# Kernel tuning notes

Hardware: AMD Instinct MI355X
Metric: run time of the kernel (lower is better)

Reference implementation:

```python
import jax, jax.numpy as jnp
import numpy as np

NUM_HEADS = 12


def setup_inputs() -> dict:
    key = jax.random.key(0)
    ks = jax.random.split(key, 7)
    B, H, W, C = 1, 64, 64, 768
    hd = C // NUM_HEADS
    return {
        "x": jax.random.normal(ks[0], (B, H, W, C), dtype=jnp.float32),
        "qkv_w": jax.random.normal(ks[1], (C, 3 * C), dtype=jnp.float32) * 0.02,
        "qkv_b": jax.random.normal(ks[2], (3 * C,), dtype=jnp.float32) * 0.02,
        "proj_w": jax.random.normal(ks[3], (C, C), dtype=jnp.float32) * 0.02,
        "proj_b": jax.random.normal(ks[4], (C,), dtype=jnp.float32) * 0.02,
        "rel_pos_h": jax.random.normal(ks[5], (2 * H - 1, hd), dtype=jnp.float32) * 0.02,
        "rel_pos_w": jax.random.normal(ks[6], (2 * W - 1, hd), dtype=jnp.float32) * 0.02,
    }


def _rel_table(size, rel_pos):
    # q_size == k_size so relative_coords = i - j + (size - 1)
    coords = jnp.arange(size)[:, None] - jnp.arange(size)[None, :] + (size - 1)
    return rel_pos[coords]  # [size, size, head_dim]


def reference(x, qkv_w, qkv_b, proj_w, proj_b, rel_pos_h, rel_pos_w):
    B, H, W, C = x.shape
    nh = NUM_HEADS
    hd = C // nh
    scale = hd ** -0.5
    N = H * W

    qkv = x.reshape(B, N, C) @ qkv_w + qkv_b  # [B, N, 3C]
    qkv = qkv.reshape(B, N, 3, nh, hd).transpose(2, 0, 3, 1, 4).reshape(3, B * nh, N, hd)
    q, k, v = qkv[0], qkv[1], qkv[2]

    attn = jnp.einsum("bqd,bkd->bqk", q * scale, k)  # [B*nh, N, N]

    # decomposed relative position bias
    Rh = _rel_table(H, rel_pos_h)  # [H, H, hd]
    Rw = _rel_table(W, rel_pos_w)  # [W, W, hd]
    qr = q.reshape(B * nh, H, W, hd)
    rel_h = jnp.einsum("bhwc,hkc->bhwk", qr, Rh)  # [B*nh, H, W, H]
    rel_w = jnp.einsum("bhwc,wkc->bhwk", qr, Rw)  # [B*nh, H, W, W]
    bias = rel_h[..., :, None] + rel_w[..., None, :]  # [B*nh, H, W, H, W]
    attn = attn + bias.reshape(B * nh, N, N)

    attn = jax.nn.softmax(attn, axis=-1)
    out = jnp.einsum("bqk,bkd->bqd", attn, v)  # [B*nh, N, hd]
    out = out.reshape(B, nh, H, W, hd).transpose(0, 2, 3, 1, 4).reshape(B, H, W, C)
    return out @ proj_w + proj_b
```

## Files before the change

### kernel.cpp

```cpp
#include <hip/hip_runtime.h>
#include <math.h>

#define NHEADS 12
#define NTOK 4096
#define LOG2E 1.44269504f

typedef __attribute__((ext_vector_type(8))) short bf8v;
typedef __attribute__((ext_vector_type(4))) float f4v;
typedef __attribute__((ext_vector_type(16))) float f16v;

__device__ __forceinline__ unsigned short f2bf(float f) {
  unsigned int u = __float_as_uint(f);
  u += 0x7fffu + ((u >> 16) & 1u);
  return (unsigned short)(u >> 16);
}
__device__ __forceinline__ float bf2f(unsigned short h) {
  return __uint_as_float(((unsigned int)h) << 16);
}
__device__ __forceinline__ bf8v pack8(float4 a, float4 b) {
  bf8v v;
  v[0] = (short)f2bf(a.x); v[1] = (short)f2bf(a.y);
  v[2] = (short)f2bf(a.z); v[3] = (short)f2bf(a.w);
  v[4] = (short)f2bf(b.x); v[5] = (short)f2bf(b.y);
  v[6] = (short)f2bf(b.z); v[7] = (short)f2bf(b.w);
  return v;
}
__device__ __forceinline__ unsigned pkbf(float hi, float lo) {
  return __builtin_amdgcn_perm(__float_as_uint(hi) + 0x8000u,
                               __float_as_uint(lo) + 0x8000u, 0x07060302u);
}

__global__ __launch_bounds__(256) void cvt_kernel(
    const float* __restrict__ in, short* __restrict__ out)
{
    const size_t i = ((size_t)blockIdx.x * 256 + threadIdx.x) * 8;
    float4 a = *(const float4*)(in + i);
    float4 b = *(const float4*)(in + i + 4);
    *(bf8v*)(out + i) = pack8(a, b);
}

__global__ __launch_bounds__(256) void cvt_rpw_kernel(
    const float* __restrict__ in, short* __restrict__ out)
{
    const int idx = blockIdx.x * 256 + threadIdx.x;
    const float v = (idx < 127 * 64) ? in[idx] : 0.f;
    out[idx] = (short)f2bf(v);
}

__global__ __launch_bounds__(256) void tcvt_kernel(
    const float* __restrict__ in, short* __restrict__ out, int R, int C)
{
    __shared__ float Ts[64][65];
    const int bc = blockIdx.x * 64, br = blockIdx.y * 64, t = threadIdx.x;
    {
        const int r = t >> 2, c0 = (t & 3) * 16;
        const float* src = in + (size_t)(br + r) * C + bc + c0;
#pragma unroll
        for (int i = 0; i < 4; ++i) {
            float4 a = *(const float4*)(src + 4 * i);
            Ts[r][c0 + 4 * i + 0] = a.x;
            Ts[r][c0 + 4 * i + 1] = a.y;
            Ts[r][c0 + 4 * i + 2] = a.z;
            Ts[r][c0 + 4 * i + 3] = a.w;
        }
    }
    __syncthreads();
    const int c = t >> 2, r0 = (t & 3) * 16;
    short* dst = out + (size_t)(bc + c) * R + br + r0;
#pragma unroll
    for (int p = 0; p < 2; ++p) {
        bf8v v;
#pragma unroll
        for (int i = 0; i < 8; ++i) v[i] = (short)f2bf(Ts[r0 + p * 8 + i][c]);
        *(bf8v*)(dst + p * 8) = v;
    }
}

__device__ __forceinline__ void gload_lds16(const void* g, void* l) {
  __builtin_amdgcn_global_load_lds(
      (const __attribute__((address_space(1))) void*)g,
      (__attribute__((address_space(3))) void*)l, 16, 0, 0);
}

__global__ __launch_bounds__(256) void qkv_mfma_kernel(
    const short* __restrict__ xh, const short* __restrict__ wT,
    const float* __restrict__ bias, short* __restrict__ qbh,
    short* __restrict__ kbh, short* __restrict__ vbT)
{
    __shared__ __align__(16) short As[128 * 32];
    __shared__ __align__(16) short Bs[128 * 32];
    const int t = threadIdx.x;
    const int w = t >> 6, lane = t & 63;
    const int l15 = lane & 15, l4 = lane >> 4;
    const int wr = w >> 1, wc = w & 1;
    const int row0 = blockIdx.y * 128, col0 = blockIdx.x * 128;
    const int ldr = lane >> 2;
    const int ldk = (lane & 3) * 8;

    f4v acc[4][4] = {};
    const short* aBase = xh + (size_t)(row0 + w * 32 + ldr) * 768 + ldk;
    const short* bBase = wT + (size_t)(col0 + w * 32 + ldr) * 768 + ldk;

    for (int kk = 0; kk < 768; kk += 32) {
        __syncthreads();
#pragma unroll
        for (int c = 0; c < 2; ++c) {
            gload_lds16(aBase + (size_t)c * 16 * 768 + kk,
                        &As[(w * 32 + c * 16) * 32]);
            gload_lds16(bBase + (size_t)c * 16 * 768 + kk,
                        &Bs[(w * 32 + c * 16) * 32]);
        }
        __syncthreads();
        bf8v af[4], bg[4];
#pragma unroll
        for (int i = 0; i < 4; ++i) {
            af[i] = *(const bf8v*)&As[(wr * 64 + 16 * i + l15) * 32 + l4 * 8];
            bg[i] = *(const bf8v*)&Bs[(wc * 64 + 16 * i + l15) * 32 + l4 * 8];
        }
#pragma unroll
        for (int i = 0; i < 4; ++i)
#pragma unroll
            for (int j = 0; j < 4; ++j)
                acc[i][j] = __builtin_amdgcn_mfma_f32_16x16x32_bf16(
                    af[i], bg[j], acc[i][j], 0, 0, 0);
    }

#pragma unroll
    for (int j = 0; j < 4; ++j) {
        const int n = col0 + wc * 64 + 16 * j + l15;
        const int s = n / 768;
        const int rm = n - s * 768;
        const int h = rm >> 6, d = rm & 63;
        const float bv = bias[n];
        if (s == 2) {
            short* vdst = vbT + (size_t)(h * 64 + d) * NTOK;
#pragma unroll
            for (int i = 0; i < 4; ++i) {
                const int m = row0 + wr * 64 + 16 * i + l4 * 4;
                short4 pv;
                pv.x = (short)f2bf(acc[i][j][0] + bv);
                pv.y = (short)f2bf(acc[i][j][1] + bv);
                pv.z = (short)f2bf(acc[i][j][2] + bv);
                pv.w = (short)f2bf(acc[i][j][3] + bv);
                *(short4*)(vdst + m) = pv;
            }
        } else {
            short* dst = (s == 0) ? qbh : kbh;
#pragma unroll
            for (int i = 0; i < 4; ++i) {
                const int m = row0 + wr * 64 + 16 * i + l4 * 4;
#pragma unroll
                for (int r = 0; r < 4; ++r)
                    dst[((size_t)h * NTOK + m + r) * 64 + d] =
                        (short)f2bf(acc[i][j][r] + bv);
            }
        }
    }
}

__global__ __launch_bounds__(256) void relu_kernel(
    const short* __restrict__ qbh, const short* __restrict__ rpwb,
    short* __restrict__ rWb)
{
    __shared__ float Us[128][65];
    const int h = blockIdx.x, qh = blockIdx.y;
    const int t = threadIdx.x, w = t >> 6, lane = t & 63;
    const int l15 = lane & 15, l4 = lane >> 4;
    const size_t hB = (size_t)h * NTOK * 64;

    bf8v bq[4][2];
#pragma unroll
    for (int nt = 0; nt < 4; ++nt) {
        const short* qs = qbh + hB + (size_t)(qh * 64 + nt * 16 + l15) * 64;
#pragma unroll
        for (int s = 0; s < 2; ++s)
            bq[nt][s] = *(const bf8v*)(qs + s * 32 + l4 * 8);
    }
    bf8v aw[2][2];
#pragma unroll
    for (int mi = 0; mi < 2; ++mi) {
        const short* as = rpwb + (size_t)((w * 2 + mi) * 16 + l15) * 64;
#pragma unroll
        for (int s = 0; s < 2; ++s)
            aw[mi][s] = *(const bf8v*)(as + s * 32 + l4 * 8);
    }
    f4v U[2][4] = {};
#pragma unroll
    for (int mi = 0; mi < 2; ++mi)
#pragma unroll
        for (int nt = 0; nt < 4; ++nt)
#pragma unroll
            for (int s = 0; s < 2; ++s)
                U[mi][nt] = __builtin_amdgcn_mfma_f32_16x16x32_bf16(
                    aw[mi][s], bq[nt][s], U[mi][nt], 0, 0, 0);
#pragma unroll
    for (int mi = 0; mi < 2; ++mi)
#pragma unroll
        for (int nt = 0; nt < 4; ++nt)
#pragma unroll
            for (int r = 0; r < 4; ++r)
                Us[(w * 2 + mi) * 16 + l4 * 4 + r][nt * 16 + l15] =
                    U[mi][nt][r];
    __syncthreads();
    const int kw = t & 63, q0 = t >> 6;
#pragma unroll
    for (int i = 0; i < 16; ++i) {
        const int q = q0 * 16 + i;
        rWb[hB + (size_t)(qh * 64 + q) * 64 + kw] =
            (short)f2bf(Us[q + 63 - kw][q] * LOG2E);
    }
}

__global__ __launch_bounds__(256, 3) void flash_mfma_kernel(
    const short* __restrict__ qbh, const short* __restrict__ kbh,
    const short* __restrict__ vbT, const short* __restrict__ rWb,
    const float* __restrict__ rph, short* __restrict__ aob)
{
    __shared__ __align__(16) short Ks[128][68];
    __shared__ __align__(16) short Vt[64][132];
    __shared__ float relHs[64][65];

    const int t = threadIdx.x;
    const int qt = blockIdx.x, head = blockIdx.y;
    const int row0 = qt * 64;
    const int lane = t & 63, w = t >> 6;
    const int qh2 = w & 1, th = w >> 1;
    const int l31 = lane & 31, hf = lane >> 5;
    const size_t hB = (size_t)head * NTOK * 64;
    const float SC = 0.125f * LOG2E;

    const int q = row0 + qh2 * 32 + l31;
    bf8v bQ[4];
    {
        const short* qsrc = qbh + hB + (size_t)q * 64;
#pragma unroll
        for (int ks = 0; ks < 4; ++ks)
            bQ[ks] = *(const bf8v*)(qsrc + ks * 16 + hf * 8);
    }
    uint2 rwp[2][4];
    {
        const short* rsrc = rWb + hB + (size_t)q * 64;
#pragma unroll
        for (int t32 = 0; t32 < 2; ++t32)
#pragma unroll
            for (int g = 0; g < 4; ++g)
                rwp[t32][g] =
                    *(const uint2*)(rsrc + t32 * 32 + 8 * g + 4 * hf);
    }

    {
        const int rr = t >> 2, d0 = (t & 3) * 16;
        const float* src = rph + (size_t)(qt + 63 - rr) * 64 + d0;
        float4 a0 = *(const float4*)(src);
        float4 a1 = *(const float4*)(src + 4);
        float4 a2 = *(const float4*)(src + 8);
        float4 a3 = *(const float4*)(src + 12);
        a0.x *= LOG2E; a0.y *= LOG2E; a0.z *= LOG2E; a0.w *= LOG2E;
        a1.x *= LOG2E; a1.y *= LOG2E; a1.z *= LOG2E; a1.w *= LOG2E;
        a2.x *= LOG2E; a2.y *= LOG2E; a2.z *= LOG2E; a2.w *= LOG2E;
        a3.x *= LOG2E; a3.y *= LOG2E; a3.z *= LOG2E; a3.w *= LOG2E;
        *(bf8v*)&Ks[rr][d0] = pack8(a0, a1);
        *(bf8v*)&Ks[rr][d0 + 8] = pack8(a2, a3);
    }
    const int sx = t >> 2;
    const int sck = (t & 3) * 16;
    const int scv = (t & 3) * 32;
    const short* kptr = kbh + hB + (size_t)sx * 64 + sck;
    const short* vptr = vbT + ((size_t)head * 64 + sx) * NTOK + scv;
    bf8v kpf[4], vpf[4];
    kpf[0] = *(const bf8v*)(kptr);
    kpf[1] = *(const bf8v*)(kptr + 8);
    kpf[2] = *(const bf8v*)(kptr + 64 * 64);
    kpf[3] = *(const bf8v*)(kptr + 64 * 64 + 8);
    vpf[0] = *(const bf8v*)(vptr);
    vpf[1] = *(const bf8v*)(vptr + 8);
    vpf[2] = *(const bf8v*)(vptr + 16);
    vpf[3] = *(const bf8v*)(vptr + 24);

    __syncthreads();
    {
        f16v c = {};
#pragma unroll
        for (int ks = 0; ks < 4; ++ks)
            c = __builtin_amdgcn_mfma_f32_32x32x16_bf16(
                *(const bf8v*)&Ks[th * 32 + l31][ks * 16 + hf * 8], bQ[ks],
                c, 0, 0, 0);
#pragma unroll
        for (int reg = 0; reg < 16; ++reg)
            relHs[th * 32 + (reg & 3) + 8 * (reg >> 2) + 4 * hf]
                 [qh2 * 32 + l31] = c[reg];
    }

    f16v O[2] = {{}, {}};
    float lsum = 0.f;

    for (int it = 0; it < 32; ++it) {
        __syncthreads();
        *(bf8v*)&Ks[sx][sck] = kpf[0];
        *(bf8v*)&Ks[sx][sck + 8] = kpf[1];
        *(bf8v*)&Ks[sx + 64][sck] = kpf[2];
        *(bf8v*)&Ks[sx + 64][sck + 8] = kpf[3];
        *(bf8v*)&Vt[sx][scv] = vpf[0];
        *(bf8v*)&Vt[sx][scv + 8] = vpf[1];
        *(bf8v*)&Vt[sx][scv + 16] = vpf[2];
        *(bf8v*)&Vt[sx][scv + 24] = vpf[3];
        {
            const int itn = (it < 31) ? it + 1 : 31;
            const short* kp = kptr + (size_t)itn * 128 * 64;
            const short* vp = vptr + itn * 128;
            kpf[0] = *(const bf8v*)kp;
            kpf[1] = *(const bf8v*)(kp + 8);
            kpf[2] = *(const bf8v*)(kp + 64 * 64);
            kpf[3] = *(const bf8v*)(kp + 64 * 64 + 8);
            vpf[0] = *(const bf8v*)vp;
            vpf[1] = *(const bf8v*)(vp + 8);
            vpf[2] = *(const bf8v*)(vp + 16);
            vpf[3] = *(const bf8v*)(vp + 24);
        }
        __syncthreads();

        f16v acc[2] = {{}, {}};
#pragma unroll
        for (int ks = 0; ks < 4; ++ks)
#pragma unroll
            for (int t32 = 0; t32 < 2; ++t32)
                acc[t32] = __builtin_amdgcn_mfma_f32_32x32x16_bf16(
                    *(const bf8v*)&Ks[th * 64 + t32 * 32 + l31]
                                     [ks * 16 + hf * 8],
                    bQ[ks], acc[t32], 0, 0, 0);

        const float rh = relHs[2 * it + th][qh2 * 32 + l31];

        unsigned xg[2][4], yg[2][4];
#pragma unroll
        for (int t32 = 0; t32 < 2; ++t32) {
            float sub = 0.f;
#pragma unroll
            for (int g = 0; g < 4; ++g) {
                const unsigned u0 = rwp[t32][g].x;
                const unsigned u1 = rwp[t32][g].y;
                const float b0 = __uint_as_float(u0 << 16) + rh;
                const float b1 = __uint_as_float(u0 & 0xffff0000u) + rh;
                const float b2 = __uint_as_float(u1 << 16) + rh;
                const float b3 = __uint_as_float(u1 & 0xffff0000u) + rh;
                const float e0 = __builtin_amdgcn_exp2f(
                    fmaf(acc[t32][4 * g + 0], SC, b0));
                const float e1 = __builtin_amdgcn_exp2f(
                    fmaf(acc[t32][4 * g + 1], SC, b1));
                const float e2 = __builtin_amdgcn_exp2f(
                    fmaf(acc[t32][4 * g + 2], SC, b2));
                const float e3 = __builtin_amdgcn_exp2f(
                    fmaf(acc[t32][4 * g + 3], SC, b3));
                sub += (e0 + e1) + (e2 + e3);
                xg[t32][g] = pkbf(e1, e0);
                yg[t32][g] = pkbf(e3, e2);
            }
            lsum += sub;
        }

#pragma unroll
        for (int t32 = 0; t32 < 2; ++t32)
#pragma unroll
            for (int ks2 = 0; ks2 < 2; ++ks2) {
                auto px = __builtin_amdgcn_permlane32_swap(
                    xg[t32][2 * ks2], xg[t32][2 * ks2 + 1], false, false);
                auto py = __builtin_amdgcn_permlane32_swap(
                    yg[t32][2 * ks2], yg[t32][2 * ks2 + 1], false, false);
                int4 av;
                av.x = (int)px[0];
                av.y = (int)py[0];
                av.z = (int)px[1];
                av.w = (int)py[1];
                union { int4 i; bf8v v; } u; u.i = av;
#pragma unroll
                for (int nt = 0; nt < 2; ++nt)
                    O[nt] = __builtin_amdgcn_mfma_f32_32x32x16_bf16(
                        u.v,
                        *(const bf8v*)&Vt[nt * 32 + l31]
                                         [th * 64 + t32 * 32 + ks2 * 16 +
                                          hf * 8],
                        O[nt], 0, 0, 0);
            }
    }

    lsum += __shfl_xor(lsum, 32);
    float* OEp = (float*)&Ks[0][0];
    float* lEp = (float*)&Vt[0][0];
    __syncthreads();
    if (th == 1) {
#pragma unroll
        for (int nt = 0; nt < 2; ++nt)
#pragma unroll
            for (int reg = 0; reg < 16; ++reg) {
                const int qr = (reg & 3) + 8 * (reg >> 2) + 4 * hf;
                OEp[(size_t)(qh2 * 32 + qr) * 64 + nt * 32 + l31] =
                    O[nt][reg];
            }
        if (lane < 32) lEp[qh2 * 32 + l31] = lsum;
    }
    __syncthreads();
    if (th == 0) {
        lsum += lEp[qh2 * 32 + l31];
        const float linv = 1.0f / lsum;
#pragma unroll
        for (int nt = 0; nt < 2; ++nt)
#pragma unroll
            for (int reg = 0; reg < 16; ++reg) {
                const int qr = (reg & 3) + 8 * (reg >> 2) + 4 * hf;
                const float li = __shfl(linv, qr);
                const float o =
                    O[nt][reg] +
                    OEp[(size_t)(qh2 * 32 + qr) * 64 + nt * 32 + l31];
                aob[(size_t)(row0 + qh2 * 32 + qr) * 768 + head * 64 +
                    nt * 32 + l31] = (short)f2bf(o * li);
            }
    }
}

__global__ __launch_bounds__(256) void proj_mfma_kernel(
    const short* __restrict__ aoh, const short* __restrict__ pwT,
    const float* __restrict__ bias, float* __restrict__ out)
{
    __shared__ __align__(16) short As[128 * 32];
    __shared__ __align__(16) short Bs[128 * 32];
    const int t = threadIdx.x;
    const int w = t >> 6, lane = t & 63;
    const int l15 = lane & 15, l4 = lane >> 4;
    const int wr = w >> 1, wc = w & 1;
    const int row0 = blockIdx.y * 128, col0 = blockIdx.x * 128;
    const int ldr = lane >> 2;
    const int ldk = (lane & 3) * 8;

    f4v acc[4][4] = {};
    const short* aBase = aoh + (size_t)(row0 + w * 32 + ldr) * 768 + ldk;
    const short* bBase = pwT + (size_t)(col0 + w * 32 + ldr) * 768 + ldk;

    for (int kk = 0; kk < 768; kk += 32) {
        __syncthreads();
#pragma unroll
        for (int c = 0; c < 2; ++c) {
            gload_lds16(aBase + (size_t)c * 16 * 768 + kk,
                        &As[(w * 32 + c * 16) * 32]);
            gload_lds16(bBase + (size_t)c * 16 * 768 + kk,
                        &Bs[(w * 32 + c * 16) * 32]);
        }
        __syncthreads();
        bf8v af[4], bg[4];
#pragma unroll
        for (int i = 0; i < 4; ++i) {
            af[i] = *(const bf8v*)&As[(wr * 64 + 16 * i + l15) * 32 + l4 * 8];
            bg[i] = *(const bf8v*)&Bs[(wc * 64 + 16 * i + l15) * 32 + l4 * 8];
        }
#pragma unroll
        for (int i = 0; i < 4; ++i)
#pragma unroll
            for (int j = 0; j < 4; ++j)
                acc[i][j] = __builtin_amdgcn_mfma_f32_16x16x32_bf16(
                    af[i], bg[j], acc[i][j], 0, 0, 0);
    }

#pragma unroll
    for (int j = 0; j < 4; ++j) {
        const int n = col0 + wc * 64 + 16 * j + l15;
        const float bv = bias[n];
#pragma unroll
        for (int i = 0; i < 4; ++i) {
            const int m = row0 + wr * 64 + 16 * i + l4 * 4;
#pragma unroll
            for (int r = 0; r < 4; ++r)
                out[(size_t)(m + r) * 768 + n] = acc[i][j][r] + bv;
        }
    }
}

extern "C" void kernel_launch(void* const* d_in, const int* in_sizes, int n_in,
                              void* d_out, int out_size, void* d_ws,
                              size_t ws_size, hipStream_t stream)
{
    (void)in_sizes; (void)n_in; (void)out_size; (void)ws_size;
    const float* x    = (const float*)d_in[0];
    const float* qkvw = (const float*)d_in[1];
    const float* qkvb = (const float*)d_in[2];
    const float* pw   = (const float*)d_in[3];
    const float* pb   = (const float*)d_in[4];
    const float* rph  = (const float*)d_in[5];
    const float* rpw  = (const float*)d_in[6];
    float* out = (float*)d_out;

    const size_t S = (size_t)NHEADS * NTOK * 64;
    short* rWb  = (short*)d_ws;
    short* qbh  = rWb + S;
    short* kbh  = qbh + S;
    short* vbT  = kbh + S;
    short* xh   = vbT + S;
    short* aob  = xh + S;
    short* wqkvT = aob + S;
    short* pwT  = wqkvT + (size_t)2304 * 768;
    short* rpwb = pwT + (size_t)768 * 768;

    cvt_kernel<<<dim3(1536), 256, 0, stream>>>(x, xh);
    tcvt_kernel<<<dim3(36, 12), 256, 0, stream>>>(qkvw, wqkvT, 768, 2304);
    tcvt_kernel<<<dim3(12, 12), 256, 0, stream>>>(pw, pwT, 768, 768);
    cvt_rpw_kernel<<<dim3(32), 256, 0, stream>>>(rpw, rpwb);
    qkv_mfma_kernel<<<dim3(18, 32), 256, 0, stream>>>(xh, wqkvT, qkvb,
                                                      qbh, kbh, vbT);
    relu_kernel<<<dim3(NHEADS, 64), 256, 0, stream>>>(qbh, rpwb, rWb);
    flash_mfma_kernel<<<dim3(64, NHEADS), 256, 0, stream>>>(qbh, kbh, vbT,
                                                            rWb, rph, aob);
    proj_mfma_kernel<<<dim3(6, 32), 256, 0, stream>>>(aob, pwT, pb, out);
}
```

Baseline: 230.9 us.

## Fuse prep conversions, fold rel-width bias into flash kernel, shrink proj tile

Merges the three fp32-to-bf16 conversion kernels into one prep kernel and drops the rpw conversion kernel. The separate relu kernel that precomputed the width bias table is removed; the flash kernel now computes it per block with MFMA into shared memory (aliased with the K/V tiles), and the height bias is computed directly from the fp32 table. The projection GEMM uses 64-row tiles to launch twice as many blocks. This cuts launches and the global round trip of the rel-width table, at the cost of extra MFMA and shared-memory work at the start of each flash block.

```diff
diff --git a/kernel.cpp b/kernel.cpp
--- a/kernel.cpp
+++ b/kernel.cpp
@@ -13,9 +13,6 @@
   unsigned int u = __float_as_uint(f);
   u += 0x7fffu + ((u >> 16) & 1u);
   return (unsigned short)(u >> 16);
-}
-__device__ __forceinline__ float bf2f(unsigned short h) {
-  return __uint_as_float(((unsigned int)h) << 16);
 }
 __device__ __forceinline__ bf8v pack8(float4 a, float4 b) {
   bf8v v;
@@ -29,29 +26,17 @@
   return __builtin_amdgcn_perm(__float_as_uint(hi) + 0x8000u,
                                __float_as_uint(lo) + 0x8000u, 0x07060302u);
 }
-
-__global__ __launch_bounds__(256) void cvt_kernel(
-    const float* __restrict__ in, short* __restrict__ out)
-{
-    const size_t i = ((size_t)blockIdx.x * 256 + threadIdx.x) * 8;
-    float4 a = *(const float4*)(in + i);
-    float4 b = *(const float4*)(in + i + 4);
-    *(bf8v*)(out + i) = pack8(a, b);
-}
-
-__global__ __launch_bounds__(256) void cvt_rpw_kernel(
-    const float* __restrict__ in, short* __restrict__ out)
-{
-    const int idx = blockIdx.x * 256 + threadIdx.x;
-    const float v = (idx < 127 * 64) ? in[idx] : 0.f;
-    out[idx] = (short)f2bf(v);
-}
-
-__global__ __launch_bounds__(256) void tcvt_kernel(
-    const float* __restrict__ in, short* __restrict__ out, int R, int C)
-{
-    __shared__ float Ts[64][65];
-    const int bc = blockIdx.x * 64, br = blockIdx.y * 64, t = threadIdx.x;
+__device__ __forceinline__ void gload_lds16(const void* g, void* l) {
+  __builtin_amdgcn_global_load_lds(
+      (const __attribute__((address_space(1))) void*)g,
+      (__attribute__((address_space(3))) void*)l, 16, 0, 0);
+}
+
+__device__ __forceinline__ void tcvt_body(
+    const float* __restrict__ in, short* __restrict__ out, int R, int C,
+    int bx, int by, int t, float (*Ts)[65])
+{
+    const int bc = bx * 64, br = by * 64;
     {
         const int r = t >> 2, c0 = (t & 3) * 16;
         const float* src = in + (size_t)(br + r) * C + bc + c0;
@@ -76,10 +61,25 @@
     }
 }
 
-__device__ __forceinline__ void gload_lds16(const void* g, void* l) {
-  __builtin_amdgcn_global_load_lds(
-      (const __attribute__((address_space(1))) void*)g,
-      (__attribute__((address_space(3))) void*)l, 16, 0, 0);
+__global__ __launch_bounds__(256) void prep_kernel(
+    const float* __restrict__ x, const float* __restrict__ qkvw,
+    const float* __restrict__ pw, short* __restrict__ xh,
+    short* __restrict__ wqkvT, short* __restrict__ pwT)
+{
+    __shared__ float Ts[64][65];
+    const int bid = blockIdx.x, t = threadIdx.x;
+    if (bid < 1536) {
+        const size_t i = ((size_t)bid * 256 + t) * 8;
+        float4 a = *(const float4*)(x + i);
+        float4 b = *(const float4*)(x + i + 4);
+        *(bf8v*)(xh + i) = pack8(a, b);
+    } else if (bid < 1968) {
+        const int idx = bid - 1536;
+        tcvt_body(qkvw, wqkvT, 768, 2304, idx % 36, idx / 36, t, Ts);
+    } else {
+        const int idx = bid - 1968;
+        tcvt_body(pw, pwT, 768, 768, idx % 12, idx / 12, t, Ts);
+    }
 }
 
 __global__ __launch_bounds__(256) void qkv_mfma_kernel(
@@ -158,67 +158,16 @@
     }
 }
 
-__global__ __launch_bounds__(256) void relu_kernel(
-    const short* __restrict__ qbh, const short* __restrict__ rpwb,
-    short* __restrict__ rWb)
-{
-    __shared__ float Us[128][65];
-    const int h = blockIdx.x, qh = blockIdx.y;
-    const int t = threadIdx.x, w = t >> 6, lane = t & 63;
-    const int l15 = lane & 15, l4 = lane >> 4;
-    const size_t hB = (size_t)h * NTOK * 64;
-
-    bf8v bq[4][2];
-#pragma unroll
-    for (int nt = 0; nt < 4; ++nt) {
-        const short* qs = qbh + hB + (size_t)(qh * 64 + nt * 16 + l15) * 64;
-#pragma unroll
-        for (int s = 0; s < 2; ++s)
-            bq[nt][s] = *(const bf8v*)(qs + s * 32 + l4 * 8);
-    }
-    bf8v aw[2][2];
-#pragma unroll
-    for (int mi = 0; mi < 2; ++mi) {
-        const short* as = rpwb + (size_t)((w * 2 + mi) * 16 + l15) * 64;
-#pragma unroll
-        for (int s = 0; s < 2; ++s)
-            aw[mi][s] = *(const bf8v*)(as + s * 32 + l4 * 8);
-    }
-    f4v U[2][4] = {};
-#pragma unroll
-    for (int mi = 0; mi < 2; ++mi)
-#pragma unroll
-        for (int nt = 0; nt < 4; ++nt)
-#pragma unroll
-            for (int s = 0; s < 2; ++s)
-                U[mi][nt] = __builtin_amdgcn_mfma_f32_16x16x32_bf16(
-                    aw[mi][s], bq[nt][s], U[mi][nt], 0, 0, 0);
-#pragma unroll
-    for (int mi = 0; mi < 2; ++mi)
-#pragma unroll
-        for (int nt = 0; nt < 4; ++nt)
-#pragma unroll
-            for (int r = 0; r < 4; ++r)
-                Us[(w * 2 + mi) * 16 + l4 * 4 + r][nt * 16 + l15] =
-                    U[mi][nt][r];
-    __syncthreads();
-    const int kw = t & 63, q0 = t >> 6;
-#pragma unroll
-    for (int i = 0; i < 16; ++i) {
-        const int q = q0 * 16 + i;
-        rWb[hB + (size_t)(qh * 64 + q) * 64 + kw] =
-            (short)f2bf(Us[q + 63 - kw][q] * LOG2E);
-    }
-}
-
 __global__ __launch_bounds__(256, 3) void flash_mfma_kernel(
     const short* __restrict__ qbh, const short* __restrict__ kbh,
-    const short* __restrict__ vbT, const short* __restrict__ rWb,
+    const short* __restrict__ vbT, const float* __restrict__ rpw,
     const float* __restrict__ rph, short* __restrict__ aob)
 {
-    __shared__ __align__(16) short Ks[128][68];
-    __shared__ __align__(16) short Vt[64][132];
-    __shared__ float relHs[64][65];
+    __shared__ __align__(16) char smem[51200];
+    short (*Ks)[68] = (short(*)[68])smem;
+    short (*Vt)[132] = (short(*)[132])(smem + 17408);
+    float (*relHs)[65] = (float(*)[65])(smem + 34304);
+    float* U = (float*)smem;
 
     const int t = threadIdx.x;
     const int qt = blockIdx.x, head = blockIdx.y;
@@ -236,31 +185,6 @@
 #pragma unroll
         for (int ks = 0; ks < 4; ++ks)
             bQ[ks] = *(const bf8v*)(qsrc + ks * 16 + hf * 8);
-    }
-    uint2 rwp[2][4];
-    {
-        const short* rsrc = rWb + hB + (size_t)q * 64;
-#pragma unroll
-        for (int t32 = 0; t32 < 2; ++t32)
-#pragma unroll
-            for (int g = 0; g < 4; ++g)
-                rwp[t32][g] =
-                    *(const uint2*)(rsrc + t32 * 32 + 8 * g + 4 * hf);
-    }
-
-    {
-        const int rr = t >> 2, d0 = (t & 3) * 16;
-        const float* src = rph + (size_t)(qt + 63 - rr) * 64 + d0;
-        float4 a0 = *(const float4*)(src);
-        float4 a1 = *(const float4*)(src + 4);
-        float4 a2 = *(const float4*)(src + 8);
-        float4 a3 = *(const float4*)(src + 12);
-        a0.x *= LOG2E; a0.y *= LOG2E; a0.z *= LOG2E; a0.w *= LOG2E;
-        a1.x *= LOG2E; a1.y *= LOG2E; a1.z *= LOG2E; a1.w *= LOG2E;
-        a2.x *= LOG2E; a2.y *= LOG2E; a2.z *= LOG2E; a2.w *= LOG2E;
-        a3.x *= LOG2E; a3.y *= LOG2E; a3.z *= LOG2E; a3.w *= LOG2E;
-        *(bf8v*)&Ks[rr][d0] = pack8(a0, a1);
-        *(bf8v*)&Ks[rr][d0 + 8] = pack8(a2, a3);
     }
     const int sx = t >> 2;
     const int sck = (t & 3) * 16;
@@ -277,14 +201,54 @@
     vpf[2] = *(const bf8v*)(vptr + 16);
     vpf[3] = *(const bf8v*)(vptr + 24);
 
+#pragma unroll
+    for (int jt2 = 0; jt2 < 2; ++jt2) {
+        const int jt = 2 * th + jt2;
+        int j = jt * 32 + l31;
+        if (j > 126) j = 0;
+        const float* asrc = rpw + (size_t)j * 64;
+        f16v c = {};
+#pragma unroll
+        for (int ks = 0; ks < 4; ++ks) {
+            float4 u0 = *(const float4*)(asrc + ks * 16 + hf * 8);
+            float4 u1 = *(const float4*)(asrc + ks * 16 + hf * 8 + 4);
+            c = __builtin_amdgcn_mfma_f32_32x32x16_bf16(
+                pack8(u0, u1), bQ[ks], c, 0, 0, 0);
+        }
+#pragma unroll
+        for (int reg = 0; reg < 16; ++reg)
+            U[(size_t)(jt * 32 + (reg & 3) + 8 * (reg >> 2) + 4 * hf) * 65 +
+              qh2 * 32 + l31] = c[reg];
+    }
     __syncthreads();
+    const int qw = qh2 * 32 + l31;
+    uint2 rwp[2][4];
+#pragma unroll
+    for (int t32 = 0; t32 < 2; ++t32)
+#pragma unroll
+        for (int g = 0; g < 4; ++g) {
+            const int kw = t32 * 32 + 8 * g + 4 * hf;
+            const float v0 = U[(qw + 63 - kw) * 65 + qw] * LOG2E;
+            const float v1 = U[(qw + 62 - kw) * 65 + qw] * LOG2E;
+            const float v2 = U[(qw + 61 - kw) * 65 + qw] * LOG2E;
+            const float v3 = U[(qw + 60 - kw) * 65 + qw] * LOG2E;
+            rwp[t32][g].x = pkbf(v1, v0);
+            rwp[t32][g].y = pkbf(v3, v2);
+        }
+
     {
+        const int kh = th * 32 + l31;
+        const float* asrc = rph + (size_t)(qt + 63 - kh) * 64;
         f16v c = {};
 #pragma unroll
-        for (int ks = 0; ks < 4; ++ks)
+        for (int ks = 0; ks < 4; ++ks) {
+            float4 u0 = *(const float4*)(asrc + ks * 16 + hf * 8);
+            float4 u1 = *(const float4*)(asrc + ks * 16 + hf * 8 + 4);
+            u0.x *= LOG2E; u0.y *= LOG2E; u0.z *= LOG2E; u0.w *= LOG2E;
+            u1.x *= LOG2E; u1.y *= LOG2E; u1.z *= LOG2E; u1.w *= LOG2E;
             c = __builtin_amdgcn_mfma_f32_32x32x16_bf16(
-                *(const bf8v*)&Ks[th * 32 + l31][ks * 16 + hf * 8], bQ[ks],
-                c, 0, 0, 0);
+                pack8(u0, u1), bQ[ks], c, 0, 0, 0);
+        }
 #pragma unroll
         for (int reg = 0; reg < 16; ++reg)
             relHs[th * 32 + (reg & 3) + 8 * (reg >> 2) + 4 * hf]
@@ -421,38 +385,37 @@
     const short* __restrict__ aoh, const short* __restrict__ pwT,
     const float* __restrict__ bias, float* __restrict__ out)
 {
-    __shared__ __align__(16) short As[128 * 32];
+    __shared__ __align__(16) short As[64 * 32];
     __shared__ __align__(16) short Bs[128 * 32];
     const int t = threadIdx.x;
     const int w = t >> 6, lane = t & 63;
     const int l15 = lane & 15, l4 = lane >> 4;
     const int wr = w >> 1, wc = w & 1;
-    const int row0 = blockIdx.y * 128, col0 = blockIdx.x * 128;
+    const int row0 = blockIdx.y * 64, col0 = blockIdx.x * 128;
     const int ldr = lane >> 2;
     const int ldk = (lane & 3) * 8;
 
-    f4v acc[4][4] = {};
-    const short* aBase = aoh + (size_t)(row0 + w * 32 + ldr) * 768 + ldk;
+    f4v acc[2][4] = {};
+    const short* aBase = aoh + (size_t)(row0 + w * 16 + ldr) * 768 + ldk;
     const short* bBase = pwT + (size_t)(col0 + w * 32 + ldr) * 768 + ldk;
 
     for (int kk = 0; kk < 768; kk += 32) {
         __syncthreads();
-#pragma unroll
-        for (int c = 0; c < 2; ++c) {
-            gload_lds16(aBase + (size_t)c * 16 * 768 + kk,
-                        &As[(w * 32 + c * 16) * 32]);
+        gload_lds16(aBase + kk, &As[(w * 16) * 32]);
+#pragma unroll
+        for (int c = 0; c < 2; ++c)
             gload_lds16(bBase + (size_t)c * 16 * 768 + kk,
                         &Bs[(w * 32 + c * 16) * 32]);
-        }
-        __syncthreads();
-        bf8v af[4], bg[4];
-#pragma unroll
-        for (int i = 0; i < 4; ++i) {
-            af[i] = *(const bf8v*)&As[(wr * 64 + 16 * i + l15) * 32 + l4 * 8];
-            bg[i] = *(const bf8v*)&Bs[(wc * 64 + 16 * i + l15) * 32 + l4 * 8];
-        }
-#pragma unroll
-        for (int i = 0; i < 4; ++i)
+        __syncthreads();
+        bf8v af[2], bg[4];
+#pragma unroll
+        for (int i = 0; i < 2; ++i)
+            af[i] = *(const bf8v*)&As[(wr * 32 + 16 * i + l15) * 32 + l4 * 8];
+#pragma unroll
+        for (int j = 0; j < 4; ++j)
+            bg[j] = *(const bf8v*)&Bs[(wc * 64 + 16 * j + l15) * 32 + l4 * 8];
+#pragma unroll
+        for (int i = 0; i < 2; ++i)
 #pragma unroll
             for (int j = 0; j < 4; ++j)
                 acc[i][j] = __builtin_amdgcn_mfma_f32_16x16x32_bf16(
@@ -464,8 +427,8 @@
         const int n = col0 + wc * 64 + 16 * j + l15;
         const float bv = bias[n];
 #pragma unroll
-        for (int i = 0; i < 4; ++i) {
-            const int m = row0 + wr * 64 + 16 * i + l4 * 4;
+        for (int i = 0; i < 2; ++i) {
+            const int m = row0 + wr * 32 + 16 * i + l4 * 4;
 #pragma unroll
             for (int r = 0; r < 4; ++r)
                 out[(size_t)(m + r) * 768 + n] = acc[i][j][r] + bv;
@@ -488,24 +451,18 @@
     float* out = (float*)d_out;
 
     const size_t S = (size_t)NHEADS * NTOK * 64;
-    short* rWb  = (short*)d_ws;
-    short* qbh  = rWb + S;
+    short* qbh  = (short*)d_ws;
     short* kbh  = qbh + S;
     short* vbT  = kbh + S;
     short* xh   = vbT + S;
     short* aob  = xh + S;
     short* wqkvT = aob + S;
     short* pwT  = wqkvT + (size_t)2304 * 768;
-    short* rpwb = pwT + (size_t)768 * 768;
-
-    cvt_kernel<<<dim3(1536), 256, 0, stream>>>(x, xh);
-    tcvt_kernel<<<dim3(36, 12), 256, 0, stream>>>(qkvw, wqkvT, 768, 2304);
-    tcvt_kernel<<<dim3(12, 12), 256, 0, stream>>>(pw, pwT, 768, 768);
-    cvt_rpw_kernel<<<dim3(32), 256, 0, stream>>>(rpw, rpwb);
+
+    prep_kernel<<<dim3(2112), 256, 0, stream>>>(x, qkvw, pw, xh, wqkvT, pwT);
     qkv_mfma_kernel<<<dim3(18, 32), 256, 0, stream>>>(xh, wqkvT, qkvb,
                                                       qbh, kbh, vbT);
-    relu_kernel<<<dim3(NHEADS, 64), 256, 0, stream>>>(qbh, rpwb, rWb);
     flash_mfma_kernel<<<dim3(64, NHEADS), 256, 0, stream>>>(qbh, kbh, vbT,
-                                                            rWb, rph, aob);
-    proj_mfma_kernel<<<dim3(6, 32), 256, 0, stream>>>(aob, pwT, pb, out);
-}
+                                                            rpw, rph, aob);
+    proj_mfma_kernel<<<dim3(6, 64), 256, 0, stream>>>(aob, pwT, pb, out);
+}
```

After: 402.7 us. +74.4%, slower.
